# Optimization experiments

Hardware: AMD Instinct MI355X
Metric: run time of the kernel (lower is better)

Reference implementation:

```python
import jax, jax.numpy as jnp
import numpy as np

NH = 8        # num_heads
KS = 64       # key_size
C_IN = 256
C_OUT = 3 * NH * KS   # 1536
GROUPS = 3 * NH       # 24
EPS = 1e-5
H = W = 64


def setup_inputs() -> dict:
    key = jax.random.key(0)
    k1, k2 = jax.random.split(key)
    x = jax.random.normal(k1, (1, C_IN, H, W), dtype=jnp.float32)
    conv_w = jax.random.normal(k2, (C_OUT, C_IN, 1, 1), dtype=jnp.float32) * 0.05
    gn_w = jnp.ones((C_OUT,), dtype=jnp.float32)
    gn_b = jnp.zeros((C_OUT,), dtype=jnp.float32)
    return {"x": x, "conv_w": conv_w, "gn_w": gn_w, "gn_b": gn_b}


def reference(x, conv_w, gn_w, gn_b):
    B, _, h, w = x.shape
    # 1x1 conv (normalize=True -> no bias): per-pixel GEMM over channels
    attn = jnp.einsum('bchw,oc->bohw', x, conv_w[:, :, 0, 0])  # [B, 1536, H, W]
    # GroupNorm: 24 groups of KS channels, normalized over (KS, H, W)
    g = attn.reshape(B, GROUPS, -1)
    mean = g.mean(axis=-1, keepdims=True)
    var = g.var(axis=-1, keepdims=True)
    g = (g - mean) * jax.lax.rsqrt(var + EPS)
    attn = g.reshape(B, C_OUT, h, w) * gn_w[None, :, None, None] + gn_b[None, :, None, None]
    # split into key, query, value (in that order, per chunk(3, dim=2))
    attn = attn.reshape(B, NH, 3 * KS, h * w)
    key_, query, value = jnp.split(attn, 3, axis=2)   # each [B, NH, KS, HW]
    # saliency = q^T @ k / sqrt(KS) -> [B, NH, HW, HW]
    saliency = jnp.einsum('bnkq,bnkl->bnql', query, key_) / jnp.sqrt(jnp.float32(KS))
    mask = jax.nn.softmax(saliency, axis=-1)
    # out = v @ mask^T -> [B, NH, KS, HW]
    out = jnp.einsum('bnkl,bnql->bnkq', value, mask)
    return out.reshape(B, NH * KS, h, w)
```

## Files before the change

### kernel.cpp

```cpp
#include <hip/hip_runtime.h>

typedef __bf16 bf16;
typedef __bf16 bf16x8 __attribute__((ext_vector_type(8)));
typedef __bf16 bf16x4 __attribute__((ext_vector_type(4)));
typedef float f32x4 __attribute__((ext_vector_type(4)));


#define QF 0.18033688011112042f

__global__ void k_misc(const float* __restrict__ x, const float* __restrict__ w,
                       bf16* __restrict__ xT, bf16* __restrict__ wb, float* __restrict__ cs) {
    int b = blockIdx.x;
    if (b < 512) {
        int t = b * 256 + threadIdx.x;
        int p  = t & 4095;
        int c0 = (t >> 12) * 8;
        bf16x8 o;
#pragma unroll
        for (int j = 0; j < 8; j++) o[j] = (bf16)x[(c0 + j) * 4096 + p];
        *(bf16x8*)(xT + p * 256 + c0) = o;
    } else if (b < 896) {
        int idx = ((b - 512) * 256 + threadIdx.x) * 4;
        float4 f = *(const float4*)(w + idx);
        bf16x4 o;
        o[0] = (bf16)f.x; o[1] = (bf16)f.y; o[2] = (bf16)f.z; o[3] = (bf16)f.w;
        *(bf16x4*)(wb + idx) = o;
    } else {
#pragma unroll
        for (int i = 0; i < 12; i++) cs[i * 256 + threadIdx.x] = 0.f;
    }
}

__global__ __launch_bounds__(256) void k_conv(const bf16* __restrict__ Wb,
                                              const bf16* __restrict__ xT,
                                              bf16* __restrict__ qkvT,
                                              float* __restrict__ cs) {
    __shared__ __attribute__((aligned(16))) bf16 tile[64 * 72];
    int wid = threadIdx.x >> 6, lane = threadIdx.x & 63;
    int quad = lane >> 4, l15 = lane & 15;
    int g  = blockIdx.x % 24;
    int pb = (blockIdx.x / 24) * 64;
    int h = g / 3, sec = g % 3;
    int ob = g * 64;
    int orow = ob + wid * 16 + l15;

    f32x4 acc[4];
#pragma unroll
    for (int c = 0; c < 4; c++) acc[c] = (f32x4){0.f, 0.f, 0.f, 0.f};

#pragma unroll
    for (int ks = 0; ks < 8; ks++) {
        bf16x8 a = *(const bf16x8*)(Wb + orow * 256 + ks * 32 + quad * 8);
#pragma unroll
        for (int c = 0; c < 4; c++) {
            bf16x8 b = *(const bf16x8*)(xT + (pb + c * 16 + l15) * 256 + ks * 32 + quad * 8);
            acc[c] = __builtin_amdgcn_mfma_f32_16x16x32_bf16(a, b, acc[c], 0, 0, 0);
        }
    }

    int ch0 = wid * 16 + quad * 4;
#pragma unroll
    for (int r = 0; r < 4; r++) {
        float sp  = acc[0][r] + acc[1][r] + acc[2][r] + acc[3][r];
        float ssp = acc[0][r] * acc[0][r] + acc[1][r] * acc[1][r]
                  + acc[2][r] * acc[2][r] + acc[3][r] * acc[3][r];
#pragma unroll
        for (int m = 1; m < 16; m <<= 1) {
            sp  += __shfl_xor(sp,  m, 64);
            ssp += __shfl_xor(ssp, m, 64);
        }
        if (l15 == 0) {
            atomicAdd(cs + (ob + ch0 + r) * 2,     sp);
            atomicAdd(cs + (ob + ch0 + r) * 2 + 1, ssp);
        }
    }

    if (sec == 2) {
#pragma unroll
        for (int c = 0; c < 4; c++)
#pragma unroll
            for (int r = 0; r < 4; r++)
                tile[(ch0 + r) * 72 + c * 16 + l15] = (bf16)acc[c][r];
    } else {
#pragma unroll
        for (int c = 0; c < 4; c++) {
            bf16x4 o;
#pragma unroll
            for (int r = 0; r < 4; r++) o[r] = (bf16)acc[c][r];
            *(bf16x4*)(&tile[(c * 16 + l15) * 72 + ch0]) = o;
        }
    }
    __syncthreads();
    bf16* base = qkvT + h * 786432;
    int t = threadIdx.x;
    if (sec == 2) {
        bf16* V = base + 524288;
#pragma unroll
        for (int it = 0; it < 2; it++) {
            int e = it * 256 + t; int ch = e >> 3; int pxo = (e & 7) * 8;
            *(bf16x8*)(V + ch * 4096 + pb + pxo) = *(const bf16x8*)(&tile[ch * 72 + pxo]);
        }
    } else {
        bf16* dst = base + (sec == 0 ? 262144 : 0);
#pragma unroll
        for (int it = 0; it < 2; it++) {
            int e = it * 256 + t; int px = e >> 3; int cho = (e & 7) * 8;
            *(bf16x8*)(dst + (pb + px) * 64 + cho) = *(const bf16x8*)(&tile[px * 72 + cho]);
        }
    }
}

__global__ __launch_bounds__(256, 2) void k_attn(const bf16* __restrict__ qkvT,
                                                 const float2* __restrict__ cs,
                                                 const float* __restrict__ gnw,
                                                 const float* __restrict__ gnb,
                                                 bf16* __restrict__ Opart,
                                                 float* __restrict__ Lsum) {
    int bid   = blockIdx.x;
    int h     = bid & 7;
    int qb    = (bid >> 3) & 15;
    int split = bid >> 7;
    int wid = threadIdx.x >> 6, lane = threadIdx.x & 63;
    int quad = lane >> 4, l15 = lane & 15;
    const bf16* QT = qkvT + h * 786432;
    const bf16* KT = QT + 262144;
    const bf16* V  = QT + 524288;
    int qw = qb * 256 + wid * 64;

    __shared__ __attribute__((aligned(16))) bf16 Ks[64 * 72];
    __shared__ __attribute__((aligned(16))) bf16 Vs[64 * 72];
    __shared__ __attribute__((aligned(16))) bf16 Ps[4][64 * 72];

    float2 vq = cs[(h * 3 + 1) * 64 + lane];
    float2 vk = cs[(h * 3 + 0) * 64 + lane];
    float sq = vq.x, ssq = vq.y, sk = vk.x, ssk = vk.y;
#pragma unroll
    for (int m = 1; m < 64; m <<= 1) {
        sq += __shfl_xor(sq, m, 64); ssq += __shfl_xor(ssq, m, 64);
        sk += __shfl_xor(sk, m, 64); ssk += __shfl_xor(ssk, m, 64);
    }
    const float N = 262144.0f;
    float mq = sq / N, iq = rsqrtf(ssq / N - mq * mq + 1e-5f);
    float mk = sk / N, ik = rsqrtf(ssk / N - mk * mk + 1e-5f);

    int r0   = threadIdx.x >> 3;
    int koff = (threadIdx.x & 7) * 8;
    float akc[8], bkc[8];
#pragma unroll
    for (int j = 0; j < 8; j++) {
        float gw = gnw[h * 192 + koff + j];
        akc[j] = ik * gw;
        bkc[j] = gnb[h * 192 + koff + j] - mk * akc[j];
    }

    bf16x8 bq[4][2];
#pragma unroll
    for (int ks = 0; ks < 2; ks++) {
        float aqc[8], bqc[8];
#pragma unroll
        for (int j = 0; j < 8; j++) {
            int ch = h * 192 + 64 + ks * 32 + quad * 8 + j;
            float gw = gnw[ch];
            aqc[j] = iq * gw * QF;
            bqc[j] = (gnb[ch] - mq * iq * gw) * QF;
        }
#pragma unroll
        for (int qs = 0; qs < 4; qs++) {
            bf16x8 raw = *(const bf16x8*)(QT + (qw + qs * 16 + l15) * 64 + ks * 32 + quad * 8);
            bf16x8 o;
#pragma unroll
            for (int j = 0; j < 8; j++) o[j] = (bf16)(aqc[j] * (float)raw[j] + bqc[j]);
            bq[qs][ks] = o;
        }
    }

    bf16x8 ones;
#pragma unroll
    for (int j = 0; j < 8; j++) ones[j] = (bf16)1.0f;

    f32x4 oacc[4][4];
#pragma unroll
    for (int c = 0; c < 4; c++)
#pragma unroll
        for (int qs = 0; qs < 4; qs++) oacc[c][qs] = (f32x4){0.f, 0.f, 0.f, 0.f};
    f32x4 oL[4];
#pragma unroll
    for (int qs = 0; qs < 4; qs++) oL[qs] = (f32x4){0.f, 0.f, 0.f, 0.f};

    int t0 = split * 16, t1 = t0 + 16;

    bf16x8 kf0, kf1, vf0, vf1;
    {
        int lb0 = t0 * 64;
        kf0 = *(const bf16x8*)(KT + (lb0 + r0) * 64 + koff);
        kf1 = *(const bf16x8*)(KT + (lb0 + r0 + 32) * 64 + koff);
        vf0 = *(const bf16x8*)(V + r0 * 4096 + lb0 + koff);
        vf1 = *(const bf16x8*)(V + (r0 + 32) * 4096 + lb0 + koff);
    }

    for (int lt = t0; lt < t1; lt++) {
        __syncthreads();
        {
            bf16x8 k0, k1;
#pragma unroll
            for (int j = 0; j < 8; j++) {
                k0[j] = (bf16)(akc[j] * (float)kf0[j] + bkc[j]);
                k1[j] = (bf16)(akc[j] * (float)kf1[j] + bkc[j]);
            }
            *(bf16x8*)(Ks + r0 * 72 + koff)        = k0;
            *(bf16x8*)(Ks + (r0 + 32) * 72 + koff) = k1;
            *(bf16x8*)(Vs + r0 * 72 + koff)        = vf0;
            *(bf16x8*)(Vs + (r0 + 32) * 72 + koff) = vf1;
        }
        __syncthreads();

        if (lt + 1 < t1) {
            int nb = (lt + 1) * 64;
            kf0 = *(const bf16x8*)(KT + (nb + r0) * 64 + koff);
            kf1 = *(const bf16x8*)(KT + (nb + r0 + 32) * 64 + koff);
            vf0 = *(const bf16x8*)(V + r0 * 4096 + nb + koff);
            vf1 = *(const bf16x8*)(V + (r0 + 32) * 4096 + nb + koff);
        }

        bf16x8 ak[2][4];
#pragma unroll
        for (int ks = 0; ks < 2; ks++)
#pragma unroll
            for (int lb = 0; lb < 4; lb++)
                ak[ks][lb] = *(const bf16x8*)(Ks + (lb * 16 + l15) * 72 + ks * 32 + quad * 8);
        bf16x8 av[2][4];
#pragma unroll
        for (int ks = 0; ks < 2; ks++)
#pragma unroll
            for (int c = 0; c < 4; c++)
                av[ks][c] = *(const bf16x8*)(Vs + (c * 16 + l15) * 72 + ks * 32 + quad * 8);

#pragma unroll
        for (int qs = 0; qs < 4; qs++) {
            f32x4 s[4];
#pragma unroll
            for (int lb = 0; lb < 4; lb++) s[lb] = (f32x4){0.f, 0.f, 0.f, 0.f};
#pragma unroll
            for (int ks = 0; ks < 2; ks++)
#pragma unroll
                for (int lb = 0; lb < 4; lb++)
                    s[lb] = __builtin_amdgcn_mfma_f32_16x16x32_bf16(ak[ks][lb], bq[qs][ks], s[lb], 0, 0, 0);
#pragma unroll
            for (int lb = 0; lb < 4; lb++) {
                bf16x4 pk;
                pk[0] = (bf16)__builtin_amdgcn_exp2f(s[lb][0]);
                pk[1] = (bf16)__builtin_amdgcn_exp2f(s[lb][1]);
                pk[2] = (bf16)__builtin_amdgcn_exp2f(s[lb][2]);
                pk[3] = (bf16)__builtin_amdgcn_exp2f(s[lb][3]);
                *(bf16x4*)(&Ps[wid][(qs * 16 + l15) * 72 + lb * 16 + quad * 4]) = pk;
            }
            bf16x8 bp0 = *(const bf16x8*)(&Ps[wid][(qs * 16 + l15) * 72 + quad * 8]);
            bf16x8 bp1 = *(const bf16x8*)(&Ps[wid][(qs * 16 + l15) * 72 + 32 + quad * 8]);
            oL[qs] = __builtin_amdgcn_mfma_f32_16x16x32_bf16(ones, bp0, oL[qs], 0, 0, 0);
            oL[qs] = __builtin_amdgcn_mfma_f32_16x16x32_bf16(ones, bp1, oL[qs], 0, 0, 0);
#pragma unroll
            for (int c = 0; c < 4; c++) {
                oacc[c][qs] = __builtin_amdgcn_mfma_f32_16x16x32_bf16(av[0][c], bp0, oacc[c][qs], 0, 0, 0);
                oacc[c][qs] = __builtin_amdgcn_mfma_f32_16x16x32_bf16(av[1][c], bp1, oacc[c][qs], 0, 0, 0);
            }
        }
    }

    if (quad == 0)
#pragma unroll
        for (int qs = 0; qs < 4; qs++)
            Lsum[split * 32768 + h * 4096 + qw + qs * 16 + l15] = oL[qs][0];

    bf16* Ob = Opart + split * 2097152;
#pragma unroll
    for (int c = 0; c < 4; c++)
#pragma unroll
        for (int qs = 0; qs < 4; qs++)
#pragma unroll
            for (int r = 0; r < 4; r++)
                Ob[(h * 64 + c * 16 + quad * 4 + r) * 4096 + qw + qs * 16 + l15] = (bf16)oacc[c][qs][r];
}

__global__ void k_final(const bf16* __restrict__ Opart, const float* __restrict__ Lsum,
                        const float2* __restrict__ cs, const float* __restrict__ gnw,
                        const float* __restrict__ gnb, float* __restrict__ out) {
    int gid = blockIdx.x * 256 + threadIdx.x;
    int row = gid >> 9;
    int c8  = (gid & 511) << 3;
    int h   = row >> 6;

    int g = h * 3 + 2;
    int c = threadIdx.x & 63;
    float2 v = cs[g * 64 + c];
    float s = v.x, ss = v.y;
#pragma unroll
    for (int m = 1; m < 64; m <<= 1) { s += __shfl_xor(s, m, 64); ss += __shfl_xor(ss, m, 64); }
    const float N = 262144.0f;
    float mean = s / N;
    float inv  = rsqrtf(ss / N - mean * mean + 1e-5f);
    int gi = h * 192 + 128 + (row & 63);
    float gw = gnw[gi];
    float va = inv * gw;
    float vb = gnb[gi] - mean * inv * gw;

    float o[8] = {0, 0, 0, 0, 0, 0, 0, 0};
    float l[8] = {0, 0, 0, 0, 0, 0, 0, 0};
#pragma unroll
    for (int sp = 0; sp < 4; sp++) {
        bf16x8 vv = *(const bf16x8*)(Opart + sp * 2097152 + row * 4096 + c8);
        const float* L = Lsum + sp * 32768 + h * 4096 + c8;
        float4 l0 = *(const float4*)L;
        float4 l1 = *(const float4*)(L + 4);
#pragma unroll
        for (int j = 0; j < 8; j++) o[j] += (float)vv[j];
        l[0] += l0.x; l[1] += l0.y; l[2] += l0.z; l[3] += l0.w;
        l[4] += l1.x; l[5] += l1.y; l[6] += l1.z; l[7] += l1.w;
    }
    float4 r0, r1;
    r0.x = va * o[0] / l[0] + vb; r0.y = va * o[1] / l[1] + vb;
    r0.z = va * o[2] / l[2] + vb; r0.w = va * o[3] / l[3] + vb;
    r1.x = va * o[4] / l[4] + vb; r1.y = va * o[5] / l[5] + vb;
    r1.z = va * o[6] / l[6] + vb; r1.w = va * o[7] / l[7] + vb;
    *(float4*)(out + row * 4096 + c8)     = r0;
    *(float4*)(out + row * 4096 + c8 + 4) = r1;
}

extern "C" void kernel_launch(void* const* d_in, const int* in_sizes, int n_in,
                              void* d_out, int out_size, void* d_ws, size_t ws_size,
                              hipStream_t stream) {
    const float* x      = (const float*)d_in[0];
    const float* conv_w = (const float*)d_in[1];
    const float* gn_w   = (const float*)d_in[2];
    const float* gn_b   = (const float*)d_in[3];
    float* out = (float*)d_out;
    char* ws = (char*)d_ws;

    bf16*   qkvT  = (bf16*) (ws);
    bf16*   Opart = (bf16*) (ws + 12582912);
    bf16*   Wb    = (bf16*) (ws + 12582912);
    bf16*   xT    = (bf16*) (ws + 13369344);
    float*  Lsum  = (float*)(ws + 29360128);
    float*  cs    = (float*)(ws + 29884416);

    hipLaunchKernelGGL(k_misc,  dim3(897),  dim3(256), 0, stream, x, conv_w, xT, Wb, cs);
    hipLaunchKernelGGL(k_conv,  dim3(1536), dim3(256), 0, stream, Wb, xT, qkvT, cs);
    hipLaunchKernelGGL(k_attn,  dim3(512),  dim3(256), 0, stream, qkvT, (const float2*)cs, gn_w, gn_b, Opart, Lsum);
    hipLaunchKernelGGL(k_final, dim3(1024), dim3(256), 0, stream, Opart, Lsum, (const float2*)cs, gn_w, gn_b, out);
}
```

Before: 149.3 us.

## Switch attention to 32x32x16 MFMA with register-resident P via lane shuffles

Rewrites the attention inner loop to use 32x32x16 bf16 MFMA tiles instead of 16x16x32. The exponentiated scores are repacked into B-operand layout with cross-half lane shuffles instead of a round trip through per-wave LDS. The row sum is accumulated in scalar registers instead of through an extra MFMA against a ones vector. The aim is to remove LDS traffic and the wasted ones-MFMAs, in exchange for more shuffle and select instructions and different register pressure.

```diff
diff --git a/kernel.cpp b/kernel.cpp
--- a/kernel.cpp
+++ b/kernel.cpp
@@ -4,6 +4,7 @@
 typedef __bf16 bf16x8 __attribute__((ext_vector_type(8)));
 typedef __bf16 bf16x4 __attribute__((ext_vector_type(4)));
 typedef float f32x4 __attribute__((ext_vector_type(4)));
+typedef float f32x16 __attribute__((ext_vector_type(16)));
 
 
 #define QF 0.18033688011112042f
@@ -121,7 +122,7 @@
     int qb    = (bid >> 3) & 15;
     int split = bid >> 7;
     int wid = threadIdx.x >> 6, lane = threadIdx.x & 63;
-    int quad = lane >> 4, l15 = lane & 15;
+    int l31 = lane & 31, half = lane >> 5;
     const bf16* QT = qkvT + h * 786432;
     const bf16* KT = QT + 262144;
     const bf16* V  = QT + 524288;
@@ -129,7 +130,6 @@
 
     __shared__ __attribute__((aligned(16))) bf16 Ks[64 * 72];
     __shared__ __attribute__((aligned(16))) bf16 Vs[64 * 72];
-    __shared__ __attribute__((aligned(16))) bf16 Ps[4][64 * 72];
 
     float2 vq = cs[(h * 3 + 1) * 64 + lane];
     float2 vk = cs[(h * 3 + 0) * 64 + lane];
@@ -153,20 +153,20 @@
         bkc[j] = gnb[h * 192 + koff + j] - mk * akc[j];
     }
 
-    bf16x8 bq[4][2];
-#pragma unroll
-    for (int ks = 0; ks < 2; ks++) {
+    bf16x8 bq[2][4];
+#pragma unroll
+    for (int ks = 0; ks < 4; ks++) {
         float aqc[8], bqc[8];
 #pragma unroll
         for (int j = 0; j < 8; j++) {
-            int ch = h * 192 + 64 + ks * 32 + quad * 8 + j;
+            int ch = h * 192 + 64 + ks * 16 + half * 8 + j;
             float gw = gnw[ch];
             aqc[j] = iq * gw * QF;
             bqc[j] = (gnb[ch] - mq * iq * gw) * QF;
         }
 #pragma unroll
-        for (int qs = 0; qs < 4; qs++) {
-            bf16x8 raw = *(const bf16x8*)(QT + (qw + qs * 16 + l15) * 64 + ks * 32 + quad * 8);
+        for (int qs = 0; qs < 2; qs++) {
+            bf16x8 raw = *(const bf16x8*)(QT + (qw + qs * 32 + l31) * 64 + ks * 16 + half * 8);
             bf16x8 o;
 #pragma unroll
             for (int j = 0; j < 8; j++) o[j] = (bf16)(aqc[j] * (float)raw[j] + bqc[j]);
@@ -174,18 +174,12 @@
         }
     }
 
-    bf16x8 ones;
-#pragma unroll
-    for (int j = 0; j < 8; j++) ones[j] = (bf16)1.0f;
-
-    f32x4 oacc[4][4];
-#pragma unroll
-    for (int c = 0; c < 4; c++)
-#pragma unroll
-        for (int qs = 0; qs < 4; qs++) oacc[c][qs] = (f32x4){0.f, 0.f, 0.f, 0.f};
-    f32x4 oL[4];
-#pragma unroll
-    for (int qs = 0; qs < 4; qs++) oL[qs] = (f32x4){0.f, 0.f, 0.f, 0.f};
+    f32x16 oacc[2][2];
+#pragma unroll
+    for (int kb = 0; kb < 2; kb++)
+#pragma unroll
+        for (int qs = 0; qs < 2; qs++) oacc[kb][qs] = (f32x16)(0.0f);
+    float ls[2] = {0.f, 0.f};
 
     int t0 = split * 16, t1 = t0 + 16;
 
@@ -198,6 +192,8 @@
         vf1 = *(const bf16x8*)(V + (r0 + 32) * 4096 + lb0 + koff);
     }
 
+    union U4 { bf16x4 v; unsigned int u[2]; };
+
     for (int lt = t0; lt < t1; lt++) {
         __syncthreads();
         {
@@ -222,63 +218,75 @@
             vf1 = *(const bf16x8*)(V + (r0 + 32) * 4096 + nb + koff);
         }
 
-        bf16x8 ak[2][4];
-#pragma unroll
-        for (int ks = 0; ks < 2; ks++)
-#pragma unroll
-            for (int lb = 0; lb < 4; lb++)
-                ak[ks][lb] = *(const bf16x8*)(Ks + (lb * 16 + l15) * 72 + ks * 32 + quad * 8);
-        bf16x8 av[2][4];
-#pragma unroll
-        for (int ks = 0; ks < 2; ks++)
-#pragma unroll
-            for (int c = 0; c < 4; c++)
-                av[ks][c] = *(const bf16x8*)(Vs + (c * 16 + l15) * 72 + ks * 32 + quad * 8);
-
-#pragma unroll
-        for (int qs = 0; qs < 4; qs++) {
-            f32x4 s[4];
-#pragma unroll
-            for (int lb = 0; lb < 4; lb++) s[lb] = (f32x4){0.f, 0.f, 0.f, 0.f};
-#pragma unroll
-            for (int ks = 0; ks < 2; ks++)
-#pragma unroll
-                for (int lb = 0; lb < 4; lb++)
-                    s[lb] = __builtin_amdgcn_mfma_f32_16x16x32_bf16(ak[ks][lb], bq[qs][ks], s[lb], 0, 0, 0);
-#pragma unroll
-            for (int lb = 0; lb < 4; lb++) {
-                bf16x4 pk;
-                pk[0] = (bf16)__builtin_amdgcn_exp2f(s[lb][0]);
-                pk[1] = (bf16)__builtin_amdgcn_exp2f(s[lb][1]);
-                pk[2] = (bf16)__builtin_amdgcn_exp2f(s[lb][2]);
-                pk[3] = (bf16)__builtin_amdgcn_exp2f(s[lb][3]);
-                *(bf16x4*)(&Ps[wid][(qs * 16 + l15) * 72 + lb * 16 + quad * 4]) = pk;
-            }
-            bf16x8 bp0 = *(const bf16x8*)(&Ps[wid][(qs * 16 + l15) * 72 + quad * 8]);
-            bf16x8 bp1 = *(const bf16x8*)(&Ps[wid][(qs * 16 + l15) * 72 + 32 + quad * 8]);
-            oL[qs] = __builtin_amdgcn_mfma_f32_16x16x32_bf16(ones, bp0, oL[qs], 0, 0, 0);
-            oL[qs] = __builtin_amdgcn_mfma_f32_16x16x32_bf16(ones, bp1, oL[qs], 0, 0, 0);
-#pragma unroll
-            for (int c = 0; c < 4; c++) {
-                oacc[c][qs] = __builtin_amdgcn_mfma_f32_16x16x32_bf16(av[0][c], bp0, oacc[c][qs], 0, 0, 0);
-                oacc[c][qs] = __builtin_amdgcn_mfma_f32_16x16x32_bf16(av[1][c], bp1, oacc[c][qs], 0, 0, 0);
-            }
-        }
-    }
-
-    if (quad == 0)
-#pragma unroll
-        for (int qs = 0; qs < 4; qs++)
-            Lsum[split * 32768 + h * 4096 + qw + qs * 16 + l15] = oL[qs][0];
+        bf16x8 ak[2][4], av[2][4];
+#pragma unroll
+        for (int ksx = 0; ksx < 4; ksx++)
+#pragma unroll
+            for (int b2 = 0; b2 < 2; b2++) {
+                ak[b2][ksx] = *(const bf16x8*)(Ks + (b2 * 32 + l31) * 72 + ksx * 16 + half * 8);
+                av[b2][ksx] = *(const bf16x8*)(Vs + (b2 * 32 + l31) * 72 + ksx * 16 + half * 8);
+            }
+
+#pragma unroll
+        for (int qs = 0; qs < 2; qs++) {
+            f32x16 s0 = (f32x16)(0.0f), s1 = (f32x16)(0.0f);
+#pragma unroll
+            for (int ks = 0; ks < 4; ks++) {
+                s0 = __builtin_amdgcn_mfma_f32_32x32x16_bf16(ak[0][ks], bq[qs][ks], s0, 0, 0, 0);
+                s1 = __builtin_amdgcn_mfma_f32_32x32x16_bf16(ak[1][ks], bq[qs][ks], s1, 0, 0, 0);
+            }
+            float e0[16], e1[16];
+#pragma unroll
+            for (int i = 0; i < 16; i++) { e0[i] = __builtin_amdgcn_exp2f(s0[i]); ls[qs] += e0[i]; }
+#pragma unroll
+            for (int i = 0; i < 16; i++) { e1[i] = __builtin_amdgcn_exp2f(s1[i]); ls[qs] += e1[i]; }
+
+            bf16x8 pf[4];
+#pragma unroll
+            for (int gp = 0; gp < 4; gp++) {
+                const float* e = (gp < 2) ? (gp & 1 ? e1 - 8 : e0) : (gp & 1 ? e1 : e0);
+                const float* eb = (gp == 0) ? e0 : (gp == 1) ? e0 + 8 : (gp == 2) ? e1 : e1 + 8;
+                U4 lo4, hi4;
+                lo4.v[0] = (bf16)eb[0]; lo4.v[1] = (bf16)eb[1];
+                lo4.v[2] = (bf16)eb[2]; lo4.v[3] = (bf16)eb[3];
+                hi4.v[0] = (bf16)eb[4]; hi4.v[1] = (bf16)eb[5];
+                hi4.v[2] = (bf16)eb[6]; hi4.v[3] = (bf16)eb[7];
+                unsigned int xlo0 = (unsigned int)__shfl_xor((int)lo4.u[0], 32, 64);
+                unsigned int xlo1 = (unsigned int)__shfl_xor((int)lo4.u[1], 32, 64);
+                unsigned int xhi0 = (unsigned int)__shfl_xor((int)hi4.u[0], 32, 64);
+                unsigned int xhi1 = (unsigned int)__shfl_xor((int)hi4.u[1], 32, 64);
+                union { bf16x8 v; unsigned int u[4]; } f;
+                f.u[0] = half ? xhi0 : lo4.u[0];
+                f.u[1] = half ? xhi1 : lo4.u[1];
+                f.u[2] = half ? hi4.u[0] : xlo0;
+                f.u[3] = half ? hi4.u[1] : xlo1;
+                pf[gp] = f.v;
+            }
+#pragma unroll
+            for (int ksl = 0; ksl < 4; ksl++) {
+                oacc[0][qs] = __builtin_amdgcn_mfma_f32_32x32x16_bf16(av[0][ksl], pf[ksl], oacc[0][qs], 0, 0, 0);
+                oacc[1][qs] = __builtin_amdgcn_mfma_f32_32x32x16_bf16(av[1][ksl], pf[ksl], oacc[1][qs], 0, 0, 0);
+            }
+        }
+    }
+
+#pragma unroll
+    for (int qs = 0; qs < 2; qs++) {
+        ls[qs] += __shfl_xor(ls[qs], 32, 64);
+        if (half == 0)
+            Lsum[split * 32768 + h * 4096 + qw + qs * 32 + l31] = ls[qs];
+    }
 
     bf16* Ob = Opart + split * 2097152;
 #pragma unroll
-    for (int c = 0; c < 4; c++)
-#pragma unroll
-        for (int qs = 0; qs < 4; qs++)
-#pragma unroll
-            for (int r = 0; r < 4; r++)
-                Ob[(h * 64 + c * 16 + quad * 4 + r) * 4096 + qw + qs * 16 + l15] = (bf16)oacc[c][qs][r];
+    for (int kb = 0; kb < 2; kb++)
+#pragma unroll
+        for (int qs = 0; qs < 2; qs++)
+#pragma unroll
+            for (int r = 0; r < 16; r++) {
+                int kd = kb * 32 + (r & 3) + 8 * (r >> 2) + 4 * half;
+                Ob[(h * 64 + kd) * 4096 + qw + qs * 32 + l31] = (bf16)oacc[kb][qs][r];
+            }
 }
 
 __global__ void k_final(const bf16* __restrict__ Opart, const float* __restrict__ Lsum,
```

Result: slower. 174.5 us (+16.8%).
